# Kernel tuning notes

Hardware: AMD Instinct MI355X
Metric: run time of the kernel (lower is better)

The kernel has to match this reference:

```python
import jax, jax.numpy as jnp
import numpy as np
from jax import lax

NT, TL = 32, 64           # num_trajs, traj_length
H, W, C = 84, 84, 4       # Atari frame stack
SIZE = 256                # LSTM hidden size
NOUT = 18                 # num_outputs
FEAT = 6 * 6 * 32         # after four stride-2 SAME convs: 84->42->21->11->6
DN = ('NHWC', 'HWIO', 'NHWC')


def setup_inputs() -> dict:
    key = jax.random.key(0)
    ks = jax.random.split(key, 8)
    d = {}
    d['inputs'] = jax.random.normal(ks[0], (NT * TL, H, W, C), jnp.float32)
    cin = C
    for i in range(4):
        d[f'w{i+1}'] = jax.random.normal(ks[1 + i], (3, 3, cin, 32), jnp.float32) * 0.1
        d[f'b{i+1}'] = jnp.zeros((32,), jnp.float32)
        cin = 32
    d['lstm_w'] = jax.random.normal(ks[5], (FEAT + SIZE, 4 * SIZE), jnp.float32) * 0.05
    d['lstm_b'] = jnp.zeros((4 * SIZE,), jnp.float32)
    d['fc_w'] = jax.random.normal(ks[6], (SIZE, NOUT), jnp.float32) * 0.01
    d['fc_b'] = jnp.zeros((NOUT,), jnp.float32)
    d['c0'] = jnp.zeros((NT, SIZE), jnp.float32)
    d['h0'] = jnp.zeros((NT, SIZE), jnp.float32)
    return d


def reference(inputs, w1, b1, w2, b2, w3, b3, w4, b4,
              lstm_w, lstm_b, fc_w, fc_b, c0, h0):
    x = inputs
    for w, b in ((w1, b1), (w2, b2), (w3, b3), (w4, b4)):
        x = jax.nn.elu(lax.conv_general_dilated(
            x, w, window_strides=(2, 2), padding='SAME',
            dimension_numbers=DN) + b)
    # [NT*TL, 6, 6, 32] -> [TL, NT, FEAT] (time-major for scan)
    xs = x.reshape(NT, TL, FEAT).transpose(1, 0, 2)

    def step(carry, xt):
        c, h = carry
        gates = jnp.concatenate([xt, h], axis=-1) @ lstm_w + lstm_b
        i, j, f, o = jnp.split(gates, 4, axis=-1)
        # BasicLSTMCell with forget_bias = 1.0
        new_c = c * jax.nn.sigmoid(f + 1.0) + jax.nn.sigmoid(i) * jnp.tanh(j)
        new_h = jnp.tanh(new_c) * jax.nn.sigmoid(o)
        return (new_c, new_h), new_h

    _, outs = lax.scan(step, (c0, h0), xs)          # outs: [TL, NT, SIZE]
    feats = outs.transpose(1, 0, 2).reshape(-1, SIZE)  # batch-major flatten
    logits = feats @ fc_w + fc_b                    # [NT*TL, NOUT]
    return logits
```

## Files before the change

### kernel.cpp

```cpp
#include <hip/hip_runtime.h>
#include <math.h>

#define NTRAJ 32
#define TLEN  64
#define BATCH (NTRAJ*TLEN)

__device__ __forceinline__ float eluf(float x){ return x > 0.f ? x : expm1f(x); }
__device__ __forceinline__ float sigmf(float x){ return 1.f/(1.f+expf(-x)); }

__global__ __launch_bounds__(256) void conv1_kernel(
    const float* __restrict__ in,
    const float* __restrict__ w,
    const float* __restrict__ b,
    float* __restrict__ out)
{
    int bid = blockIdx.x;
    bid = (bid & 7)*1764 + (bid >> 3);
    int pos = bid*256 + threadIdx.x;
    int n   = pos / (42*42);
    int rem = pos % (42*42);
    int oy  = rem / 42, ox = rem % 42;
    float acc[32];
    #pragma unroll
    for(int o=0;o<32;o++) acc[o] = b[o];
    for(int ky=0; ky<3; ky++){
        int iy = 2*oy + ky;
        if(iy >= 84) continue;
        for(int kx=0; kx<3; kx++){
            int ix = 2*ox + kx;
            if(ix >= 84) continue;
            float4 v = *(const float4*)(in + (((n*84 + iy)*84) + ix)*4);
            const float* wq = w + (ky*3 + kx)*128;
            #pragma unroll
            for(int o=0;o<32;o++) acc[o] += v.x*wq[o];
            #pragma unroll
            for(int o=0;o<32;o++) acc[o] += v.y*wq[32+o];
            #pragma unroll
            for(int o=0;o<32;o++) acc[o] += v.z*wq[64+o];
            #pragma unroll
            for(int o=0;o<32;o++) acc[o] += v.w*wq[96+o];
        }
    }
    float4* op = (float4*)(out + (size_t)pos*32);
    #pragma unroll
    for(int q=0;q<8;q++)
        op[q] = make_float4(eluf(acc[4*q]), eluf(acc[4*q+1]),
                            eluf(acc[4*q+2]), eluf(acc[4*q+3]));
}

template<int IH, int IW, int OH, int OW, int PB>
__global__ __launch_bounds__(256) void convN_kernel(
    const float* __restrict__ in,
    const float* __restrict__ w,
    const float* __restrict__ b,
    float* __restrict__ out)
{
    int bid = blockIdx.x;
    const int cpx = gridDim.x >> 3;
    bid = (bid & 7)*cpx + (bid >> 3);
    int pos = bid*256 + threadIdx.x;
    if(pos >= BATCH*OH*OW) return;
    int n   = pos / (OH*OW);
    int rem = pos % (OH*OW);
    int oy  = rem / OW, ox = rem % OW;
    float acc[32];
    #pragma unroll
    for(int o=0;o<32;o++) acc[o] = b[o];
    for(int ky=0; ky<3; ky++){
        int iy = 2*oy + ky - PB;
        if(iy < 0 || iy >= IH) continue;
        for(int kx=0; kx<3; kx++){
            int ix = 2*ox + kx - PB;
            if(ix < 0 || ix >= IW) continue;
            const float4* ip = (const float4*)(in + ((size_t)(n*IH + iy)*IW + ix)*32);
            const float* wp = w + (ky*3 + kx)*1024;
            #pragma unroll
            for(int c4=0;c4<8;c4++){
                float4 x = ip[c4];
                const float* wq = wp + c4*128;
                #pragma unroll
                for(int o=0;o<32;o++) acc[o] += x.x*wq[o];
                #pragma unroll
                for(int o=0;o<32;o++) acc[o] += x.y*wq[32+o];
                #pragma unroll
                for(int o=0;o<32;o++) acc[o] += x.z*wq[64+o];
                #pragma unroll
                for(int o=0;o<32;o++) acc[o] += x.w*wq[96+o];
            }
        }
    }
    float4* op = (float4*)(out + (size_t)pos*32);
    #pragma unroll
    for(int q=0;q<8;q++)
        op[q] = make_float4(eluf(acc[4*q]), eluf(acc[4*q+1]),
                            eluf(acc[4*q+2]), eluf(acc[4*q+3]));
}

__global__ __launch_bounds__(256) void relayout_kernel(
    const float* __restrict__ p4,
    float* __restrict__ at)
{
    int i = blockIdx.x*256 + threadIdx.x;
    int f = i >> 11, r = i & 2047;
    int tt = r >> 5, n = r & 31;
    int nt = n*64 + tt;
    at[i] = p4[nt*1152 + f];
}

__global__ __launch_bounds__(256) void gx_gemm_kernel(
    const float* __restrict__ at,
    const float* __restrict__ lw,
    const float* __restrict__ lb,
    float* __restrict__ gx,
    unsigned int* __restrict__ bar)
{
    if(blockIdx.x == 0 && blockIdx.y == 0 && threadIdx.x < 32)
        bar[threadIdx.x*32] = 0u;
    int lane = threadIdx.x & 63;
    int wv   = threadIdx.x >> 6;
    int r0   = blockIdx.x * 16;
    int oc   = blockIdx.y*256 + wv*64 + lane;
    float acc[16];
    float bias = lb[oc];
    #pragma unroll
    for(int i=0;i<16;i++) acc[i] = bias;
    #pragma unroll 4
    for(int k=0;k<1152;k++){
        float wval = lw[k*1024 + oc];
        const float* ap = at + k*2048 + r0;
        #pragma unroll
        for(int i=0;i<16;i++) acc[i] += ap[i] * wval;
    }
    #pragma unroll
    for(int i=0;i<16;i++) gx[(r0+i)*1024 + oc] = acc[i];
}

__global__ __launch_bounds__(256) void lstm_coop_kernel(
    const float* __restrict__ gx,
    const float* __restrict__ lw,
    const float* __restrict__ c0,
    const float* __restrict__ h0,
    float* __restrict__ feats,
    float* __restrict__ hbuf,
    unsigned int* __restrict__ bar)
{
    __shared__ float hs[32*256];
    __shared__ float wl2[32*256];
    float* const gl = hs;

    const int wg = blockIdx.x;
    const int t  = threadIdx.x;
    const int c    = t & 31;
    const int ngrp = t >> 5;
    const int gcol = (c>>3)*256 + wg*8 + (c&7);
    const float* wh = lw + 1152*1024;

    #pragma unroll
    for(int i=0;i<32;i++){
        int e = t + 256*i;
        int k = e >> 5, cc = e & 31;
        int gc = (cc>>3)*256 + wg*8 + (cc&7);
        wl2[(k>>1)*64 + cc*2 + (k&1)] = wh[k*1024 + gc];
    }
    const int un = t >> 3, uu = t & 7;
    float cst = c0[un*256 + wg*8 + uu];

    const float2* wv  = (const float2*)wl2;
    float4* hs4 = (float4*)hs;

    for(int st=0; st<64; ++st){
        const float4* hp4 = (const float4*)((st == 0) ? h0 : (hbuf + ((st&1)^1)*8192));
        #pragma unroll
        for(int i=0;i<8;i++){
            int q = t + 256*i;
            hs4[q] = hp4[q];
        }
        int rbase = st*32 + ngrp*4;
        float gx0 = gx[(rbase+0)*1024 + gcol];
        float gx1 = gx[(rbase+1)*1024 + gcol];
        float gx2 = gx[(rbase+2)*1024 + gcol];
        float gx3 = gx[(rbase+3)*1024 + gcol];
        __syncthreads();
        float a0 = 0.f, a1 = 0.f, a2 = 0.f, a3 = 0.f;
        const float4* h0r = hs4 + (ngrp*4+0)*64;
        const float4* h1r = hs4 + (ngrp*4+1)*64;
        const float4* h2r = hs4 + (ngrp*4+2)*64;
        const float4* h3r = hs4 + (ngrp*4+3)*64;
        #pragma unroll 4
        for(int k4=0;k4<64;k4++){
            float2 wa = wv[(2*k4+0)*32 + c];
            float2 wb = wv[(2*k4+1)*32 + c];
            float4 hv0 = h0r[k4], hv1 = h1r[k4], hv2 = h2r[k4], hv3 = h3r[k4];
            a0 += hv0.x*wa.x + hv0.y*wa.y + hv0.z*wb.x + hv0.w*wb.y;
            a1 += hv1.x*wa.x + hv1.y*wa.y + hv1.z*wb.x + hv1.w*wb.y;
            a2 += hv2.x*wa.x + hv2.y*wa.y + hv2.z*wb.x + hv2.w*wb.y;
            a3 += hv3.x*wa.x + hv3.y*wa.y + hv3.z*wb.x + hv3.w*wb.y;
        }
        __syncthreads();
        gl[(ngrp*4+0)*33 + c] = a0 + gx0;
        gl[(ngrp*4+1)*33 + c] = a1 + gx1;
        gl[(ngrp*4+2)*33 + c] = a2 + gx2;
        gl[(ngrp*4+3)*33 + c] = a3 + gx3;
        __syncthreads();
        {
            float i_ = gl[un*33 +      uu];
            float j_ = gl[un*33 +  8 + uu];
            float f_ = gl[un*33 + 16 + uu];
            float o_ = gl[un*33 + 24 + uu];
            cst = cst*sigmf(f_ + 1.f) + sigmf(i_)*tanhf(j_);
            float h = tanhf(cst)*sigmf(o_);
            int col = wg*8 + uu;
            hbuf[(st&1)*8192 + un*256 + col] = h;
            feats[(un*64 + st)*256 + col]    = h;
        }
        if(st != 63){
            __syncthreads();
            if(t == 0)
                __hip_atomic_store(bar + wg*32, (unsigned)(st+1),
                                   __ATOMIC_RELEASE, __HIP_MEMORY_SCOPE_AGENT);
            if(t < 32){
                unsigned tgt = (unsigned)(st+1);
                unsigned spins = 0;
                while(__hip_atomic_load(bar + t*32, __ATOMIC_ACQUIRE,
                                        __HIP_MEMORY_SCOPE_AGENT) < tgt){
                    __builtin_amdgcn_s_sleep(1);
                    if(++spins > 20000000u) break;
                }
            }
            __syncthreads();
        }
    }
}

__global__ __launch_bounds__(64) void fc_kernel(
    const float* __restrict__ feats, const float* __restrict__ fw,
    const float* __restrict__ fb,    float* __restrict__ out)
{
    __shared__ float h[256];
    int p = blockIdx.x, t = threadIdx.x;
    *(float4*)&h[t*4] = *(const float4*)(feats + p*256 + t*4);
    __syncthreads();
    if(t < 18){
        float acc = fb[t];
        for(int k=0;k<256;k++) acc += h[k]*fw[k*18 + t];
        out[p*18 + t] = acc;
    }
}

extern "C" void kernel_launch(void* const* d_in, const int* in_sizes, int n_in,
                              void* d_out, int out_size, void* d_ws, size_t ws_size,
                              hipStream_t stream) {
    const float* inp = (const float*)d_in[0];
    const float* w1  = (const float*)d_in[1];  const float* b1 = (const float*)d_in[2];
    const float* w2  = (const float*)d_in[3];  const float* b2 = (const float*)d_in[4];
    const float* w3  = (const float*)d_in[5];  const float* b3 = (const float*)d_in[6];
    const float* w4  = (const float*)d_in[7];  const float* b4 = (const float*)d_in[8];
    const float* lw  = (const float*)d_in[9];  const float* lb = (const float*)d_in[10];
    const float* fw  = (const float*)d_in[11]; const float* fb = (const float*)d_in[12];
    const float* c0  = (const float*)d_in[13]; const float* h0 = (const float*)d_in[14];
    float* out = (float*)d_out;
    float* ws  = (float*)d_ws;

    const size_t n1 = (size_t)32*3612672;
    const size_t n3 = (size_t)32*247808;
    const size_t n4 = (size_t)32*73728;

    float* p1 = ws;
    float* p2 = p1 + n1;
    float* p3 = ws;
    float* p4 = p3 + n3;
    float* at = p4 + n4;
    float* gxb   = at  + (size_t)1152*2048;
    float* feats = gxb + (size_t)2048*1024;
    float* hbuf  = feats + (size_t)2048*256;
    unsigned int* bar = (unsigned int*)(hbuf + 2*32*256);

    conv1_kernel<<<14112,256,0,stream>>>(inp, w1, b1, p1);
    convN_kernel<42,42,21,21,0><<<3528,256,0,stream>>>(p1, w2, b2, p2);
    convN_kernel<21,21,11,11,1><<<968,256,0,stream>>>(p2, w3, b3, p3);
    convN_kernel<11,11, 6, 6,1><<<288,256,0,stream>>>(p3, w4, b4, p4);
    relayout_kernel<<<9216,256,0,stream>>>(p4, at);
    gx_gemm_kernel<<<dim3(128,4),256,0,stream>>>(at, lw, lb, gxb, bar);
    lstm_coop_kernel<<<32,256,0,stream>>>(gxb, lw, c0, h0, feats, hbuf, bar);
    fc_kernel<<<2048,64,0,stream>>>(feats, fw, fb, out);
}
```

Baseline: 1.843 ms.

## Spread LSTM recurrence across 128 cooperative blocks with padded shared layout

The persistent LSTM kernel now runs on 128 blocks instead of 32, so each block owns 2 hidden units (8 gate columns) rather than 8. Each thread computes one dot product over 256 hidden inputs for one gate column of one trajectory. Shared arrays are padded to 260 floats per row to avoid bank conflicts. The goal is to cut the serial per-step matmul latency by spreading it over more CUs. In exchange, the grid barrier must now poll 128 flags per step, each block reloads the full h vector every step, and only 64 threads do the gate math.

```diff
diff --git a/kernel.cpp b/kernel.cpp
--- a/kernel.cpp
+++ b/kernel.cpp
@@ -114,7 +114,7 @@
     float* __restrict__ gx,
     unsigned int* __restrict__ bar)
 {
-    if(blockIdx.x == 0 && blockIdx.y == 0 && threadIdx.x < 32)
+    if(blockIdx.x == 0 && blockIdx.y == 0 && threadIdx.x < 128)
         bar[threadIdx.x*32] = 0u;
     int lane = threadIdx.x & 63;
     int wv   = threadIdx.x >> 6;
@@ -144,28 +144,27 @@
     float* __restrict__ hbuf,
     unsigned int* __restrict__ bar)
 {
-    __shared__ float hs[32*256];
-    __shared__ float wl2[32*256];
-    float* const gl = hs;
+    __shared__ float hs[32*260];
+    __shared__ float wl[8*260];
+    __shared__ float gl[32*9];
 
     const int wg = blockIdx.x;
     const int t  = threadIdx.x;
-    const int c    = t & 31;
-    const int ngrp = t >> 5;
-    const int gcol = (c>>3)*256 + wg*8 + (c&7);
+    const int n    = t >> 3;
+    const int cidx = t & 7;
+    const int gcol = (cidx>>1)*256 + wg*2 + (cidx&1);
     const float* wh = lw + 1152*1024;
 
     #pragma unroll
-    for(int i=0;i<32;i++){
+    for(int i=0;i<8;i++){
         int e = t + 256*i;
-        int k = e >> 5, cc = e & 31;
-        int gc = (cc>>3)*256 + wg*8 + (cc&7);
-        wl2[(k>>1)*64 + cc*2 + (k&1)] = wh[k*1024 + gc];
-    }
-    const int un = t >> 3, uu = t & 7;
-    float cst = c0[un*256 + wg*8 + uu];
-
-    const float2* wv  = (const float2*)wl2;
+        int k = e >> 3, cc = e & 7;
+        int gc = (cc>>1)*256 + wg*2 + (cc&1);
+        wl[cc*260 + k] = wh[k*1024 + gc];
+    }
+    const int un = t >> 1, uu = t & 1;
+    float cst = (t < 64) ? c0[un*256 + wg*2 + uu] : 0.f;
+
     float4* hs4 = (float4*)hs;
 
     for(int st=0; st<64; ++st){
@@ -173,43 +172,30 @@
         #pragma unroll
         for(int i=0;i<8;i++){
             int q = t + 256*i;
-            hs4[q] = hp4[q];
-        }
-        int rbase = st*32 + ngrp*4;
-        float gx0 = gx[(rbase+0)*1024 + gcol];
-        float gx1 = gx[(rbase+1)*1024 + gcol];
-        float gx2 = gx[(rbase+2)*1024 + gcol];
-        float gx3 = gx[(rbase+3)*1024 + gcol];
+            int row = q >> 6, col4 = q & 63;
+            hs4[row*65 + col4] = hp4[q];
+        }
+        float gxv = gx[(st*32 + n)*1024 + gcol];
         __syncthreads();
-        float a0 = 0.f, a1 = 0.f, a2 = 0.f, a3 = 0.f;
-        const float4* h0r = hs4 + (ngrp*4+0)*64;
-        const float4* h1r = hs4 + (ngrp*4+1)*64;
-        const float4* h2r = hs4 + (ngrp*4+2)*64;
-        const float4* h3r = hs4 + (ngrp*4+3)*64;
-        #pragma unroll 4
+        float a = 0.f;
+        const float4* hr = (const float4*)&hs[n*260];
+        const float4* wr = (const float4*)&wl[cidx*260];
+        #pragma unroll 8
         for(int k4=0;k4<64;k4++){
-            float2 wa = wv[(2*k4+0)*32 + c];
-            float2 wb = wv[(2*k4+1)*32 + c];
-            float4 hv0 = h0r[k4], hv1 = h1r[k4], hv2 = h2r[k4], hv3 = h3r[k4];
-            a0 += hv0.x*wa.x + hv0.y*wa.y + hv0.z*wb.x + hv0.w*wb.y;
-            a1 += hv1.x*wa.x + hv1.y*wa.y + hv1.z*wb.x + hv1.w*wb.y;
-            a2 += hv2.x*wa.x + hv2.y*wa.y + hv2.z*wb.x + hv2.w*wb.y;
-            a3 += hv3.x*wa.x + hv3.y*wa.y + hv3.z*wb.x + hv3.w*wb.y;
-        }
+            float4 hv = hr[k4];
+            float4 wv = wr[k4];
+            a += hv.x*wv.x + hv.y*wv.y + hv.z*wv.z + hv.w*wv.w;
+        }
+        gl[n*9 + cidx] = a + gxv;
         __syncthreads();
-        gl[(ngrp*4+0)*33 + c] = a0 + gx0;
-        gl[(ngrp*4+1)*33 + c] = a1 + gx1;
-        gl[(ngrp*4+2)*33 + c] = a2 + gx2;
-        gl[(ngrp*4+3)*33 + c] = a3 + gx3;
-        __syncthreads();
-        {
-            float i_ = gl[un*33 +      uu];
-            float j_ = gl[un*33 +  8 + uu];
-            float f_ = gl[un*33 + 16 + uu];
-            float o_ = gl[un*33 + 24 + uu];
+        if(t < 64){
+            float i_ = gl[un*9 +     uu];
+            float j_ = gl[un*9 + 2 + uu];
+            float f_ = gl[un*9 + 4 + uu];
+            float o_ = gl[un*9 + 6 + uu];
             cst = cst*sigmf(f_ + 1.f) + sigmf(i_)*tanhf(j_);
             float h = tanhf(cst)*sigmf(o_);
-            int col = wg*8 + uu;
+            int col = wg*2 + uu;
             hbuf[(st&1)*8192 + un*256 + col] = h;
             feats[(un*64 + st)*256 + col]    = h;
         }
@@ -218,7 +204,7 @@
             if(t == 0)
                 __hip_atomic_store(bar + wg*32, (unsigned)(st+1),
                                    __ATOMIC_RELEASE, __HIP_MEMORY_SCOPE_AGENT);
-            if(t < 32){
+            if(t < 128){
                 unsigned tgt = (unsigned)(st+1);
                 unsigned spins = 0;
                 while(__hip_atomic_load(bar + t*32, __ATOMIC_ACQUIRE,
@@ -281,6 +267,6 @@
     convN_kernel<11,11, 6, 6,1><<<288,256,0,stream>>>(p3, w4, b4, p4);
     relayout_kernel<<<9216,256,0,stream>>>(p4, at);
     gx_gemm_kernel<<<dim3(128,4),256,0,stream>>>(at, lw, lb, gxb, bar);
-    lstm_coop_kernel<<<32,256,0,stream>>>(gxb, lw, c0, h0, feats, hbuf, bar);
+    lstm_coop_kernel<<<128,256,0,stream>>>(gxb, lw, c0, h0, feats, hbuf, bar);
     fc_kernel<<<2048,64,0,stream>>>(feats, fw, fb, out);
 }
```

New measurement: 2.019 ms. 9.6% more time.
